# Kernel tuning notes

Hardware: AMD Instinct MI355X
Metric: run time of the kernel (lower is better)

Reference implementation:

```python
import jax, jax.numpy as jnp
import numpy as np

N_HEAD = 8


def setup_inputs() -> dict:
    key = jax.random.key(0)
    ks = jax.random.split(key, 5)
    D = 512
    q = jax.random.normal(ks[0], (2, 4096, D), dtype=jnp.float32)
    s = 0.02  # init scale for weights
    Wq = jax.random.normal(ks[1], (D, D), dtype=jnp.float32) * s
    Wk = jax.random.normal(ks[2], (D, D), dtype=jnp.float32) * s
    Wv = jax.random.normal(ks[3], (D, D), dtype=jnp.float32) * s
    Wo = jax.random.normal(ks[4], (D, D), dtype=jnp.float32) * s
    z = jnp.zeros((D,), dtype=jnp.float32)
    return {"q": q, "Wq": Wq, "bq": z, "Wk": Wk, "bk": z, "Wv": Wv, "bv": z, "Wo": Wo, "bo": z}


def _split_heads(x, n_head):
    # (b, s, c) -> (b, h, s, c//h)
    b, s, c = x.shape
    return x.reshape(b, s, n_head, c // n_head).transpose(0, 2, 1, 3)


def reference(q, Wq, bq, Wk, bk, Wv, bv, Wo, bo):
    # Linear projections (nn.Linear: x @ W.T + b); self-attention (kv = q)
    qp = _split_heads(q @ Wq.T + bq, N_HEAD)  # (b, h, s, dh)
    kp = _split_heads(q @ Wk.T + bk, N_HEAD)
    vp = _split_heads(q @ Wv.T + bv, N_HEAD)
    dh = qp.shape[-1]
    scale = 1.0 / jnp.sqrt(jnp.asarray(dh, dtype=qp.dtype))
    # unfused MATH-backend SDPA: full [b,h,s,s] scores, stable softmax, no dropout (eval)
    scores = jnp.einsum("bhqd,bhkd->bhqk", qp, kp) * scale
    probs = jax.nn.softmax(scores, axis=-1)
    attn = jnp.einsum("bhqk,bhkd->bhqd", probs, vp)  # (b, h, s, dh)
    # merge heads: (b, h, s, dh) -> (b, s, h*dh)
    b, h, s, _ = attn.shape
    merged = attn.transpose(0, 2, 1, 3).reshape(b, s, h * dh)
    return merged @ Wo.T + bo
```

## Files before the change

kernel.cpp:

```cpp
#include <hip/hip_runtime.h>
#include <hip/hip_bf16.h>
#include <math.h>

typedef __attribute__((ext_vector_type(8))) short bf16x8;
typedef __attribute__((ext_vector_type(4))) short bf16x4;
typedef __attribute__((ext_vector_type(4))) float f32x4;

__device__ __forceinline__ unsigned short f2bf(float f) {
    union { float f; unsigned int u; } v; v.f = f;
    unsigned int u = v.u;
    u += 0x7fffu + ((u >> 16) & 1u);
    return (unsigned short)(u >> 16);
}

__device__ __forceinline__ f32x4 mfma16(bf16x4 a, bf16x4 b, f32x4 c) {
#if __has_builtin(__builtin_amdgcn_mfma_f32_16x16x16bf16_1k)
    return __builtin_amdgcn_mfma_f32_16x16x16bf16_1k(a, b, c, 0, 0, 0);
#else
    asm volatile("v_mfma_f32_16x16x16_bf16 %0, %1, %2, %0\n\ts_nop 7"
                 : "+v"(c) : "v"(a), "v"(b));
    return c;
#endif
}

__device__ __forceinline__ unsigned packbf2(float a, float b) {
    __hip_bfloat162 h = __float22bfloat162_rn(float2{a, b});
    union { __hip_bfloat162 h; unsigned u; } v; v.h = h;
    return v.u;
}

__device__ __forceinline__ float fmax3(float a, float b, float c) {
    return fmaxf(fmaxf(a, b), c);
}

template<int A_BF16>
__device__ __forceinline__ void gemm_body(const void* Ap, const float* W,
                                          f32x4 (&acc)[4][4],
                                          unsigned short (*As)[40], unsigned short (*Bs)[40],
                                          int bm, int bn, int t)
{
    constexpr int Kdim = 512;
    const int lane = t & 63, g = lane >> 4, c = lane & 15;
    const int w = t >> 6, wr = w >> 1, wc = w & 1;

    uint4  paB[2];
    float4 paF[4];
    float4 pw[4];
    const int ccB = (t & 3) * 8, r0B = t >> 2;
    const int c4  = (t & 7) * 4, r0F = t >> 3;

    if (A_BF16) {
        const unsigned short* A = (const unsigned short*)Ap;
        for (int p = 0; p < 2; ++p)
            paB[p] = *(const uint4*)(A + (size_t)(bm + r0B + p * 64) * Kdim + ccB);
    } else {
        const float* A = (const float*)Ap;
        for (int p = 0; p < 4; ++p)
            paF[p] = *(const float4*)(A + (size_t)(bm + r0F + p * 32) * Kdim + c4);
    }
    for (int p = 0; p < 4; ++p)
        pw[p] = *(const float4*)(W + (size_t)(bn + r0F + p * 32) * Kdim + c4);

    for (int k0 = 0; k0 < Kdim; k0 += 32) {
        __syncthreads();
        if (A_BF16) {
            for (int p = 0; p < 2; ++p)
                *(uint4*)&As[r0B + p * 64][ccB] = paB[p];
        } else {
            for (int p = 0; p < 4; ++p) {
                float4 v = paF[p];
                ushort4 hv;
                hv.x = f2bf(v.x); hv.y = f2bf(v.y); hv.z = f2bf(v.z); hv.w = f2bf(v.w);
                *(ushort4*)&As[r0F + p * 32][c4] = hv;
            }
        }
        for (int p = 0; p < 4; ++p) {
            float4 v = pw[p];
            ushort4 hv;
            hv.x = f2bf(v.x); hv.y = f2bf(v.y); hv.z = f2bf(v.z); hv.w = f2bf(v.w);
            *(ushort4*)&Bs[r0F + p * 32][c4] = hv;
        }
        __syncthreads();
        if (k0 + 32 < Kdim) {
            const int kn = k0 + 32;
            if (A_BF16) {
                const unsigned short* A = (const unsigned short*)Ap;
                for (int p = 0; p < 2; ++p)
                    paB[p] = *(const uint4*)(A + (size_t)(bm + r0B + p * 64) * Kdim + kn + ccB);
            } else {
                const float* A = (const float*)Ap;
                for (int p = 0; p < 4; ++p)
                    paF[p] = *(const float4*)(A + (size_t)(bm + r0F + p * 32) * Kdim + kn + c4);
            }
            for (int p = 0; p < 4; ++p)
                pw[p] = *(const float4*)(W + (size_t)(bn + r0F + p * 32) * Kdim + kn + c4);
        }
        bf16x8 af[4], bfr[4];
        for (int i = 0; i < 4; ++i)
            af[i] = *(const bf16x8*)&As[wr * 64 + i * 16 + c][g * 8];
        for (int j = 0; j < 4; ++j)
            bfr[j] = *(const bf16x8*)&Bs[wc * 64 + j * 16 + c][g * 8];
        for (int i = 0; i < 4; ++i)
            for (int j = 0; j < 4; ++j)
                acc[i][j] = __builtin_amdgcn_mfma_f32_16x16x32_bf16(af[i], bfr[j], acc[i][j], 0, 0, 0);
    }
}

__global__ __launch_bounds__(256, 2)
void gemm_qkv(const float* __restrict__ q,
              const float* __restrict__ Wq, const float* __restrict__ bq,
              const float* __restrict__ Wk, const float* __restrict__ bk,
              const float* __restrict__ Wv, const float* __restrict__ bv,
              unsigned short* __restrict__ Qo, unsigned short* __restrict__ Ko,
              unsigned short* __restrict__ Vo)
{
    __shared__ unsigned short As[128][40];
    __shared__ unsigned short Bs[128][40];
    const int t = threadIdx.x, z = blockIdx.z;
    const int lane = t & 63, g = lane >> 4, c = lane & 15;
    const int w = t >> 6, wr = w >> 1, wc = w & 1;
    const int bm = blockIdx.x * 128, bn = blockIdx.y * 128;

    const float* W    = (z == 0) ? Wq : (z == 1) ? Wk : Wv;
    const float* bias = (z == 0) ? bq : (z == 1) ? bk : bv;
    unsigned short* Out = (z == 0) ? Qo : (z == 1) ? Ko : Vo;

    f32x4 acc[4][4] = {};
    gemm_body<0>((const void*)q, W, acc, As, Bs, bm, bn, t);

    float bv4[4];
    for (int j = 0; j < 4; ++j) bv4[j] = bias[bn + wc * 64 + j * 16 + c];
    for (int i = 0; i < 4; ++i)
        for (int j = 0; j < 4; ++j)
            for (int r = 0; r < 4; ++r) {
                int m = bm + wr * 64 + i * 16 + 4 * g + r;
                int n = bn + wc * 64 + j * 16 + c;
                float val = acc[i][j][r] + bv4[j];
                int b = m >> 12, s = m & 4095, h = n >> 6, d = n & 63;
                if (z < 2)
                    Out[((((size_t)b * 8 + h) * 4096 + s) << 6) + d] = f2bf(val);
                else
                    Out[(((size_t)b * 8 + h) * 64 + d) * 4096 + s] = f2bf(val);
            }
}

__global__ __launch_bounds__(256, 2)
void gemm_out(const unsigned short* __restrict__ A, const float* __restrict__ W,
              const float* __restrict__ bias, float* __restrict__ Out)
{
    __shared__ unsigned short As[128][40];
    __shared__ unsigned short Bs[128][40];
    const int t = threadIdx.x;
    const int lane = t & 63, g = lane >> 4, c = lane & 15;
    const int w = t >> 6, wr = w >> 1, wc = w & 1;
    const int bm = blockIdx.x * 128, bn = blockIdx.y * 128;

    f32x4 acc[4][4] = {};
    gemm_body<1>((const void*)A, W, acc, As, Bs, bm, bn, t);

    float bv4[4];
    for (int j = 0; j < 4; ++j) bv4[j] = bias[bn + wc * 64 + j * 16 + c];
    for (int i = 0; i < 4; ++i)
        for (int j = 0; j < 4; ++j)
            for (int r = 0; r < 4; ++r) {
                int m = bm + wr * 64 + i * 16 + 4 * g + r;
                int n = bn + wc * 64 + j * 16 + c;
                Out[(size_t)m * 512 + n] = acc[i][j][r] + bv4[j];
            }
}

__global__ __launch_bounds__(256, 2)
void attn128(const unsigned short* __restrict__ Q, const unsigned short* __restrict__ Kh,
             const unsigned short* __restrict__ VT, unsigned short* __restrict__ Mo)
{
    __shared__ unsigned short Ks[64 * 64];
    __shared__ unsigned short Vs[64 * 64];

    const int t = threadIdx.x, w = t >> 6, lane = t & 63, g = lane >> 4, c = lane & 15;
    const int idp = (blockIdx.x & 7) * 64 + (blockIdx.x >> 3);
    const int bh = idp >> 5;
    const int q0 = (idp & 31) * 128;
    const unsigned short* Qb = Q + (size_t)bh * 4096 * 64;
    const unsigned short* Kb = Kh + (size_t)bh * 4096 * 64;
    const unsigned short* Vb = VT + (size_t)bh * 64 * 4096;

    bf16x8 qfa0, qfa1, qfb0, qfb1;
    {
        int qra = q0 + w * 32 + c;
        qfa0 = *(const bf16x8*)(Qb + (size_t)qra * 64 + g * 8);
        qfa1 = *(const bf16x8*)(Qb + (size_t)qra * 64 + 32 + g * 8);
        qfb0 = *(const bf16x8*)(Qb + (size_t)(qra + 16) * 64 + g * 8);
        qfb1 = *(const bf16x8*)(Qb + (size_t)(qra + 16) * 64 + 32 + g * 8);
    }

    f32x4 oa[4] = {}, ob[4] = {};
    f32x4 lacca = {}, laccb = {};
    float nma = 0.f, nmb = 0.f;

    bf16x4 ones;
    ones[0] = ones[1] = ones[2] = ones[3] = (short)0x3F80;

    const int srow = t >> 2, scol = (t & 3) * 16;
    const int s0 = (t & 3) * 2, r7 = srow & 7;
    const int woff0 = srow * 64 + ((s0 ^ r7) << 3);
    const int woff1 = srow * 64 + (((s0 + 1) ^ r7) << 3);
    const unsigned short* kp0 = Kb + (size_t)srow * 64 + scol;
    const unsigned short* vp0 = Vb + (size_t)srow * 4096 + scol;

    uint4 ka0 = *(const uint4*)(kp0);
    uint4 ka1 = *(const uint4*)(kp0 + 8);
    uint4 va0 = *(const uint4*)(vp0);
    uint4 va1 = *(const uint4*)(vp0 + 8);

    const float sc2 = 0.125f * 1.44269504f;
    const float THR = 10.f;
    const int c7 = c & 7;

    for (int jt = 0; jt < 64; ++jt) {
        __syncthreads();
        *(uint4*)&Ks[woff0] = ka0;
        *(uint4*)&Ks[woff1] = ka1;
        *(uint4*)&Vs[woff0] = va0;
        *(uint4*)&Vs[woff1] = va1;
        __syncthreads();
        if (jt < 63) {
            const unsigned short* kp = kp0 + (size_t)(jt + 1) * 4096;
            ka0 = *(const uint4*)(kp);
            ka1 = *(const uint4*)(kp + 8);
            const unsigned short* vp = vp0 + (jt + 1) * 64;
            va0 = *(const uint4*)(vp);
            va1 = *(const uint4*)(vp + 8);
        }

        f32x4 ta[4], tb[4];
        #pragma unroll
        for (int nt = 0; nt < 4; ++nt) {
            int row = nt * 16 + c;
            bf16x8 kf0 = *(const bf16x8*)&Ks[row * 64 + ((g ^ c7) << 3)];
            bf16x8 kf1 = *(const bf16x8*)&Ks[row * 64 + (((4 + g) ^ c7) << 3)];
            f32x4 za = {}, zb = {};
            za = __builtin_amdgcn_mfma_f32_16x16x32_bf16(kf0, qfa0, za, 0, 0, 0);
            za = __builtin_amdgcn_mfma_f32_16x16x32_bf16(kf1, qfa1, za, 0, 0, 0);
            zb = __builtin_amdgcn_mfma_f32_16x16x32_bf16(kf0, qfb0, zb, 0, 0, 0);
            zb = __builtin_amdgcn_mfma_f32_16x16x32_bf16(kf1, qfb1, zb, 0, 0, 0);
            #pragma unroll
            for (int r = 0; r < 4; ++r) {
                ta[nt][r] = fmaf(za[r], sc2, nma);
                tb[nt][r] = fmaf(zb[r], sc2, nmb);
            }
        }

        float tma = fmax3(fmax3(fmax3(ta[0][0], ta[0][1], ta[0][2]),
                                fmax3(ta[0][3], ta[1][0], ta[1][1]),
                                fmax3(ta[1][2], ta[1][3], ta[2][0])),
                          fmax3(fmax3(ta[2][1], ta[2][2], ta[2][3]),
                                fmax3(ta[3][0], ta[3][1], ta[3][2]), ta[3][3]),
                          -3.0e38f);
        float tmb = fmax3(fmax3(fmax3(tb[0][0], tb[0][1], tb[0][2]),
                                fmax3(tb[0][3], tb[1][0], tb[1][1]),
                                fmax3(tb[1][2], tb[1][3], tb[2][0])),
                          fmax3(fmax3(tb[2][1], tb[2][2], tb[2][3]),
                                fmax3(tb[3][0], tb[3][1], tb[3][2]), tb[3][3]),
                          -3.0e38f);
        if (!__all(tma <= THR && tmb <= THR)) {
            float pma = tma, pmb = tmb;
            pma = fmaxf(pma, __shfl_xor(pma, 16));
            pma = fmaxf(pma, __shfl_xor(pma, 32));
            pmb = fmaxf(pmb, __shfl_xor(pmb, 16));
            pmb = fmaxf(pmb, __shfl_xor(pmb, 32));
            float dma = fmaxf(pma, 0.f), dmb = fmaxf(pmb, 0.f);
            nma -= dma; nmb -= dmb;
            float ala = exp2f(-dma), alb = exp2f(-dmb);
            #pragma unroll
            for (int nt = 0; nt < 4; ++nt)
                #pragma unroll
                for (int r = 0; r < 4; ++r) { ta[nt][r] -= dma; tb[nt][r] -= dmb; }
            #pragma unroll
            for (int r = 0; r < 4; ++r) {
                float ara = __shfl(ala, 4 * g + r);
                float arb = __shfl(alb, 4 * g + r);
                #pragma unroll
                for (int nd = 0; nd < 4; ++nd) { oa[nd][r] *= ara; ob[nd][r] *= arb; }
                lacca[r] *= ara; laccb[r] *= arb;
            }
        }

        bf16x4 pfa[4], pfb[4];
        #pragma unroll
        for (int nt = 0; nt < 4; ++nt) {
            union { unsigned u[2]; bf16x4 v; } pk;
            pk.u[0] = packbf2(exp2f(ta[nt][0]), exp2f(ta[nt][1]));
            pk.u[1] = packbf2(exp2f(ta[nt][2]), exp2f(ta[nt][3]));
            pfa[nt] = pk.v;
            pk.u[0] = packbf2(exp2f(tb[nt][0]), exp2f(tb[nt][1]));
            pk.u[1] = packbf2(exp2f(tb[nt][2]), exp2f(tb[nt][3]));
            pfb[nt] = pk.v;
        }

        #pragma unroll
        for (int nd = 0; nd < 4; ++nd) {
            int row = nd * 16 + c;
            #pragma unroll
            for (int nt = 0; nt < 4; ++nt) {
                int off = row * 64 + (((2 * nt + (g >> 1)) ^ c7) << 3) + ((g & 1) << 2);
                bf16x4 vf = *(const bf16x4*)&Vs[off];
                oa[nd] = mfma16(pfa[nt], vf, oa[nd]);
                ob[nd] = mfma16(pfb[nt], vf, ob[nd]);
            }
        }
        #pragma unroll
        for (int nt = 0; nt < 4; ++nt) {
            lacca = mfma16(pfa[nt], ones, lacca);
            laccb = mfma16(pfb[nt], ones, laccb);
        }
    }

    const int b = bh >> 3, h = bh & 7;
    #pragma unroll
    for (int r = 0; r < 4; ++r) {
        float inva = 1.f / lacca[r];
        float invb = 1.f / laccb[r];
        int ma = b * 4096 + q0 + w * 32 + 4 * g + r;
        #pragma unroll
        for (int nd = 0; nd < 4; ++nd) {
            int n = h * 64 + nd * 16 + c;
            Mo[(size_t)ma * 512 + n]        = f2bf(oa[nd][r] * inva);
            Mo[(size_t)(ma + 16) * 512 + n] = f2bf(ob[nd][r] * invb);
        }
    }
}

extern "C" void kernel_launch(void* const* d_in, const int* in_sizes, int n_in,
                              void* d_out, int out_size, void* d_ws, size_t ws_size,
                              hipStream_t stream) {
    const float* q  = (const float*)d_in[0];
    const float* Wq = (const float*)d_in[1];
    const float* bq = (const float*)d_in[2];
    const float* Wk = (const float*)d_in[3];
    const float* bk = (const float*)d_in[4];
    const float* Wv = (const float*)d_in[5];
    const float* bv = (const float*)d_in[6];
    const float* Wo = (const float*)d_in[7];
    const float* bo = (const float*)d_in[8];

    unsigned short* Qb = (unsigned short*)d_ws;
    unsigned short* Kb = Qb + (size_t)16 * 4096 * 64;
    unsigned short* Vt = Kb + (size_t)16 * 4096 * 64;
    unsigned short* Mg = Vt + (size_t)16 * 4096 * 64;

    dim3 gb(256);
    dim3 gqkv(64, 4, 3);
    gemm_qkv<<<gqkv, gb, 0, stream>>>(q, Wq, bq, Wk, bk, Wv, bv, Qb, Kb, Vt);

    dim3 ga(512);
    attn128<<<ga, gb, 0, stream>>>(Qb, Kb, Vt, Mg);

    dim3 gg(64, 4);
    gemm_out<<<gg, gb, 0, stream>>>(Mg, Wo, bo, (float*)d_out);
}
```

Measured before the change: 197.7 us.

## Double-buffer attention K/V tiles in LDS and fold softmax scale into Q projection

```diff
diff --git a/kernel.cpp b/kernel.cpp
--- a/kernel.cpp
+++ b/kernel.cpp
@@ -124,6 +124,7 @@
     const float* W    = (z == 0) ? Wq : (z == 1) ? Wk : Wv;
     const float* bias = (z == 0) ? bq : (z == 1) ? bk : bv;
     unsigned short* Out = (z == 0) ? Qo : (z == 1) ? Ko : Vo;
+    const float osc = (z == 0) ? 0.125f * 1.44269504f : 1.0f;
 
     f32x4 acc[4][4] = {};
     gemm_body<0>((const void*)q, W, acc, As, Bs, bm, bn, t);
@@ -135,7 +136,7 @@
             for (int r = 0; r < 4; ++r) {
                 int m = bm + wr * 64 + i * 16 + 4 * g + r;
                 int n = bn + wc * 64 + j * 16 + c;
-                float val = acc[i][j][r] + bv4[j];
+                float val = (acc[i][j][r] + bv4[j]) * osc;
                 int b = m >> 12, s = m & 4095, h = n >> 6, d = n & 63;
                 if (z < 2)
                     Out[((((size_t)b * 8 + h) * 4096 + s) << 6) + d] = f2bf(val);
@@ -173,8 +174,8 @@
 void attn128(const unsigned short* __restrict__ Q, const unsigned short* __restrict__ Kh,
              const unsigned short* __restrict__ VT, unsigned short* __restrict__ Mo)
 {
-    __shared__ unsigned short Ks[64 * 64];
-    __shared__ unsigned short Vs[64 * 64];
+    __shared__ unsigned short Ks[2 * 64 * 64];
+    __shared__ unsigned short Vs[2 * 64 * 64];
 
     const int t = threadIdx.x, w = t >> 6, lane = t & 63, g = lane >> 4, c = lane & 15;
     const int idp = (blockIdx.x & 7) * 64 + (blockIdx.x >> 3);
@@ -211,17 +212,16 @@
     uint4 ka1 = *(const uint4*)(kp0 + 8);
     uint4 va0 = *(const uint4*)(vp0);
     uint4 va1 = *(const uint4*)(vp0 + 8);
-
-    const float sc2 = 0.125f * 1.44269504f;
+    *(uint4*)&Ks[woff0] = ka0;
+    *(uint4*)&Ks[woff1] = ka1;
+    *(uint4*)&Vs[woff0] = va0;
+    *(uint4*)&Vs[woff1] = va1;
+
     const float THR = 10.f;
     const int c7 = c & 7;
 
-    for (int jt = 0; jt < 64; ++jt) {
-        __syncthreads();
-        *(uint4*)&Ks[woff0] = ka0;
-        *(uint4*)&Ks[woff1] = ka1;
-        *(uint4*)&Vs[woff0] = va0;
-        *(uint4*)&Vs[woff1] = va1;
+    auto tile_iter = [&](int jt, const unsigned short* Kc, const unsigned short* Vc,
+                         unsigned short* Kn, unsigned short* Vn) {
         __syncthreads();
         if (jt < 63) {
             const unsigned short* kp = kp0 + (size_t)(jt + 1) * 4096;
@@ -236,32 +236,28 @@
         #pragma unroll
         for (int nt = 0; nt < 4; ++nt) {
             int row = nt * 16 + c;
-            bf16x8 kf0 = *(const bf16x8*)&Ks[row * 64 + ((g ^ c7) << 3)];
-            bf16x8 kf1 = *(const bf16x8*)&Ks[row * 64 + (((4 + g) ^ c7) << 3)];
-            f32x4 za = {}, zb = {};
+            bf16x8 kf0 = *(const bf16x8*)&Kc[row * 64 + ((g ^ c7) << 3)];
+            bf16x8 kf1 = *(const bf16x8*)&Kc[row * 64 + (((4 + g) ^ c7) << 3)];
+            f32x4 za = {nma, nma, nma, nma};
+            f32x4 zb = {nmb, nmb, nmb, nmb};
             za = __builtin_amdgcn_mfma_f32_16x16x32_bf16(kf0, qfa0, za, 0, 0, 0);
             za = __builtin_amdgcn_mfma_f32_16x16x32_bf16(kf1, qfa1, za, 0, 0, 0);
             zb = __builtin_amdgcn_mfma_f32_16x16x32_bf16(kf0, qfb0, zb, 0, 0, 0);
             zb = __builtin_amdgcn_mfma_f32_16x16x32_bf16(kf1, qfb1, zb, 0, 0, 0);
-            #pragma unroll
-            for (int r = 0; r < 4; ++r) {
-                ta[nt][r] = fmaf(za[r], sc2, nma);
-                tb[nt][r] = fmaf(zb[r], sc2, nmb);
-            }
+            ta[nt] = za;
+            tb[nt] = zb;
         }
 
         float tma = fmax3(fmax3(fmax3(ta[0][0], ta[0][1], ta[0][2]),
                                 fmax3(ta[0][3], ta[1][0], ta[1][1]),
                                 fmax3(ta[1][2], ta[1][3], ta[2][0])),
-                          fmax3(fmax3(ta[2][1], ta[2][2], ta[2][3]),
-                                fmax3(ta[3][0], ta[3][1], ta[3][2]), ta[3][3]),
-                          -3.0e38f);
+                          fmax3(ta[2][1], ta[2][2], ta[2][3]),
+                          fmax3(fmax3(ta[3][0], ta[3][1], ta[3][2]), ta[3][3], ta[3][3]));
         float tmb = fmax3(fmax3(fmax3(tb[0][0], tb[0][1], tb[0][2]),
                                 fmax3(tb[0][3], tb[1][0], tb[1][1]),
                                 fmax3(tb[1][2], tb[1][3], tb[2][0])),
-                          fmax3(fmax3(tb[2][1], tb[2][2], tb[2][3]),
-                                fmax3(tb[3][0], tb[3][1], tb[3][2]), tb[3][3]),
-                          -3.0e38f);
+                          fmax3(tb[2][1], tb[2][2], tb[2][3]),
+                          fmax3(fmax3(tb[3][0], tb[3][1], tb[3][2]), tb[3][3], tb[3][3]));
         if (!__all(tma <= THR && tmb <= THR)) {
             float pma = tma, pmb = tmb;
             pma = fmaxf(pma, __shfl_xor(pma, 16));
@@ -303,7 +299,7 @@
             #pragma unroll
             for (int nt = 0; nt < 4; ++nt) {
                 int off = row * 64 + (((2 * nt + (g >> 1)) ^ c7) << 3) + ((g & 1) << 2);
-                bf16x4 vf = *(const bf16x4*)&Vs[off];
+                bf16x4 vf = *(const bf16x4*)&Vc[off];
                 oa[nd] = mfma16(pfa[nt], vf, oa[nd]);
                 ob[nd] = mfma16(pfb[nt], vf, ob[nd]);
             }
@@ -313,6 +309,18 @@
             lacca = mfma16(pfa[nt], ones, lacca);
             laccb = mfma16(pfb[nt], ones, laccb);
         }
+
+        if (jt < 63) {
+            *(uint4*)&Kn[woff0] = ka0;
+            *(uint4*)&Kn[woff1] = ka1;
+            *(uint4*)&Vn[woff0] = va0;
+            *(uint4*)&Vn[woff1] = va1;
+        }
+    };
+
+    for (int jt2 = 0; jt2 < 64; jt2 += 2) {
+        tile_iter(jt2,     &Ks[0],    &Vs[0],    &Ks[4096], &Vs[4096]);
+        tile_iter(jt2 + 1, &Ks[4096], &Vs[4096], &Ks[0],    &Vs[0]);
     }
 
     const int b = bh >> 3, h = bh & 7;
```

Measured after the change: 184.1 us. 6.9% less time.
